# Kernel optimization log

Hardware: AMD Instinct MI355X
Metric: run time of the kernel (lower is better)

Reference implementation:

```python
import jax, jax.numpy as jnp
import numpy as np

SHIFTS = [1, 2, 4]  # matches init_kwargs 'shifts' (all in range 0 < s < channels)


def setup_inputs() -> dict:
    key = jax.random.key(0)
    k1, k2, k3 = jax.random.split(key, 3)
    B, H, L, D = 4, 1, 2048, 512
    factor = 4
    proj_in = 2 * len(SHIFTS) * D  # cli_mode='full' -> 2 components per shift
    x = jax.random.normal(k1, (B, H, L, D), dtype=jnp.float32)
    W = jax.random.normal(k2, (factor, D), dtype=jnp.float32) * 0.05
    # glorot-ish scale for the projection kernel
    proj_kernel = jax.random.normal(k3, (proj_in, D), dtype=jnp.float32) * (1.0 / np.sqrt(proj_in))
    proj_bias = jnp.zeros((D,), dtype=jnp.float32)
    return {"x": x, "W": W, "proj_kernel": proj_kernel, "proj_bias": proj_bias}


def reference(x, W, proj_kernel, proj_bias):
    # x: (B, H, L, D); W: (k, D) slot multivectors
    k, D = W.shape
    B, H, L, _ = x.shape
    # coarse[-1] treated as zeros; non-anchor slots source previous coarse vector
    coarse_prev = jnp.pad(x, ((0, 0), (0, 0), (1, 0), (0, 0)))[:, :, :-1, :]
    # src: (B, H, L, k, D) — slots 0..k-2 from coarse_prev, slot k-1 (anchor) from x
    src = jnp.concatenate(
        [jnp.repeat(coarse_prev[:, :, :, None, :], k - 1, axis=3),
         x[:, :, :, None, :]],
        axis=3,
    )
    W_b = W[None, None, None, :, :]  # (1,1,1,k,D)
    components = []
    for s in SHIFTS:
        src_s = jnp.roll(src, s, axis=-1)
        W_s_b = jnp.roll(W, s, axis=-1)[None, None, None, :, :]
        sw = src * W_s_b
        components.append(sw - W_b * src_s)        # wedge part
        components.append(jax.nn.silu(sw))          # inner part (full mode)
    g = jnp.concatenate(components, axis=-1)  # (B,H,L,k, 2*len(shifts)*D)
    fine = jnp.einsum('bhlkc,cd->bhlkd', g, proj_kernel) + proj_bias
    return fine.reshape(B, H, L * k, D)
```

## Files before the change

### kernel.cpp

```cpp
#include <hip/hip_runtime.h>
#include <cstdint>
#include <cstddef>

#define D_DIM 512
#define L_DIM 2048
#define KB_DIM 2048
#define KS_DIM 1536
#define NROWS_X 2049
#define M_TOT 32768

typedef __bf16 bf16x8 __attribute__((ext_vector_type(8)));
typedef float  f32x4  __attribute__((ext_vector_type(4)));

__device__ __forceinline__ unsigned f2bf(float f) {
  unsigned u = __float_as_uint(f);
  u += 0x7FFF + ((u >> 16) & 1);
  return u >> 16;
}
__device__ __forceinline__ float bf2f(unsigned short u) {
  return __uint_as_float(((unsigned)u) << 16);
}
__device__ __forceinline__ void gld_lds16(const void* g, void* l) {
  __builtin_amdgcn_global_load_lds((const __attribute__((address_space(1))) void*)g,
                                   (__attribute__((address_space(3))) void*)l,
                                   16, 0, 0);
}

__global__ void convert_x(const float* __restrict__ x, unsigned short* __restrict__ XbfZ) {
  const int b = blockIdx.y;
  const int idx = blockIdx.x * 256 + threadIdx.x;
  if (idx >= NROWS_X * 128) return;
  const int rr = idx >> 7;
  const int c4 = idx & 127;
  uint2 p = {0u, 0u};
  if (rr > 0) {
    float4 v = reinterpret_cast<const float4*>(x)[((size_t)b * L_DIM + rr - 1) * 128 + c4];
    p.x = f2bf(v.x) | (f2bf(v.y) << 16);
    p.y = f2bf(v.z) | (f2bf(v.w) << 16);
  }
  reinterpret_cast<uint2*>(XbfZ)[((size_t)b * NROWS_X + rr) * 128 + c4] = p;
}

__global__ void build_B(const float* __restrict__ P, const float* __restrict__ W,
                        unsigned short* __restrict__ Ball,
                        unsigned short* __restrict__ Wtab, int buildWtab) {
  if (buildWtab && blockIdx.x == 0) {
    for (int i = threadIdx.x; i < 6144; i += 256) {
      const int c = i & 511; const int rest = i >> 9;
      const int si = rest % 3; const int jj = rest / 3;
      Wtab[(jj * 3 + si) * 512 + c] =
          (unsigned short)f2bf(W[jj * 512 + ((c - (1 << si)) & 511)]);
    }
  }
  const int bx = blockIdx.x;
  const int j = bx >> 6, dt = (bx >> 3) & 7, ct = bx & 7;
  const int t = threadIdx.x;
  const int d = dt * 64 + (t & 63);
  const int cbase = ct * 64 + (t >> 6) * 16;
  unsigned short bufd[16];
  unsigned short bufs[3][16];
  #pragma unroll
  for (int cc = 0; cc < 16; ++cc) {
    const int c = cbase + cc;
    float qd = 0.f;
    #pragma unroll
    for (int si = 0; si < 3; ++si) {
      const int s = 1 << si;
      const int cm = (c - s) & 511, cp = (c + s) & 511;
      qd += W[j * 512 + cm] * P[((size_t)(2 * si) * 512 + c) * 512 + d]
          - W[j * 512 + cp] * P[((size_t)(2 * si) * 512 + cp) * 512 + d];
      bufs[si][cc] = (unsigned short)f2bf(P[((size_t)(2 * si + 1) * 512 + c) * 512 + d]);
    }
    bufd[cc] = (unsigned short)f2bf(qd);
  }
  unsigned short* row = Ball + (size_t)(j * 512 + d) * KB_DIM;
  *reinterpret_cast<uint4*>(&row[cbase])     = *reinterpret_cast<uint4*>(&bufd[0]);
  *reinterpret_cast<uint4*>(&row[cbase + 8]) = *reinterpret_cast<uint4*>(&bufd[8]);
  #pragma unroll
  for (int si = 0; si < 3; ++si) {
    *reinterpret_cast<uint4*>(&row[512 + si * 512 + cbase])     = *reinterpret_cast<uint4*>(&bufs[si][0]);
    *reinterpret_cast<uint4*>(&row[512 + si * 512 + cbase + 8]) = *reinterpret_cast<uint4*>(&bufs[si][8]);
  }
}

__global__ void gs_gen(const unsigned short* __restrict__ XbfZ,
                       const unsigned short* __restrict__ Wtab,
                       unsigned short* __restrict__ GS) {
  const int m0 = blockIdx.x * 4;
  const int j = m0 >> 13, b = (m0 >> 11) & 3, lbase = m0 & 2047;
  const int r = threadIdx.x >> 6, lane = threadIdx.x & 63;
  const int l = lbase + r;
  const size_t vrow = (size_t)b * NROWS_X + l + (j == 3);
  union U { uint4 q; unsigned short s[8]; };
  U va;
  va.q = *reinterpret_cast<const uint4*>(XbfZ + vrow * 512 + lane * 8);
  unsigned short* o = GS + (size_t)(m0 + r) * KS_DIM + lane * 8;
  #pragma unroll
  for (int si = 0; si < 3; ++si) {
    U wa;
    wa.q = *reinterpret_cast<const uint4*>(Wtab + (j * 3 + si) * 512 + lane * 8);
    unsigned res[4];
    #pragma unroll
    for (int e = 0; e < 4; ++e) {
      float s0 = bf2f(va.s[2 * e])     * bf2f(wa.s[2 * e]);
      float s1 = bf2f(va.s[2 * e + 1]) * bf2f(wa.s[2 * e + 1]);
      float g0 = s0 * __builtin_amdgcn_rcpf(1.f + __expf(-s0));
      float g1 = s1 * __builtin_amdgcn_rcpf(1.f + __expf(-s1));
      res[e] = f2bf(g0) | (f2bf(g1) << 16);
    }
    uint4 ov = {res[0], res[1], res[2], res[3]};
    *reinterpret_cast<uint4*>(o + si * 512) = ov;
  }
}

__global__ __launch_bounds__(256) void gemm_main(
    const unsigned short* __restrict__ XbfZ, const unsigned short* __restrict__ GS,
    const unsigned short* __restrict__ Ball, const float* __restrict__ bias,
    float* __restrict__ out) {
  __shared__ alignas(16) unsigned short At[2][4096];
  __shared__ alignas(16) unsigned short Bt[2][4096];

  const int tid = threadIdx.x;
  const int bx = blockIdx.x;
  const int nt = bx >> 8;
  const int mt = bx & 255;
  const int j  = mt >> 6;
  const int b  = (mt >> 4) & 3;
  const int l0 = (mt & 15) * 128;
  const int n0 = nt * 128;

  const int rA = tid >> 2;
  const int qA = (tid & 3) ^ ((rA >> 2) & 3);
  const unsigned short* srcAd0 = XbfZ + (size_t)(b * NROWS_X + l0 + (j == 3) + rA) * 512 + qA * 8;
  const unsigned short* srcAd1 = srcAd0 + (size_t)64 * 512;
  const size_t mbase = (size_t)((j * 4 + b) * L_DIM + l0);
  const unsigned short* srcAs0 = GS + (mbase + rA) * KS_DIM + qA * 8;
  const unsigned short* srcAs1 = srcAs0 + (size_t)64 * KS_DIM;
  const unsigned short* srcB0 = Ball + (size_t)(j * 512 + n0 + rA) * KB_DIM + qA * 8;
  const unsigned short* srcB1 = srcB0 + (size_t)64 * KB_DIM;

  const int lane = tid & 63, wv = tid >> 6;
  const int wm = wv >> 1, wn = wv & 1;
  const int l16 = lane & 15, quad = lane >> 4;
  const int qf = quad ^ ((l16 >> 2) & 3);
  const int aBase = (wm * 64 + l16) * 32 + qf * 8;
  const int bBase = (wn * 64 + l16) * 32 + qf * 8;

  f32x4 acc[4][4];
  #pragma unroll
  for (int i = 0; i < 4; ++i)
    #pragma unroll
    for (int n = 0; n < 4; ++n)
      acc[i][n] = f32x4{0.f, 0.f, 0.f, 0.f};

  gld_lds16(srcAd0, &At[0][tid * 8]);
  gld_lds16(srcAd1, &At[0][(tid + 256) * 8]);
  gld_lds16(srcB0,  &Bt[0][tid * 8]);
  gld_lds16(srcB1,  &Bt[0][(tid + 256) * 8]);

  for (int it = 0; it < 64; ++it) {
    const int buf = it & 1;
    __syncthreads();
    if (it + 1 < 64) {
      const int nx = it + 1, nb = buf ^ 1;
      const unsigned short *a0, *a1;
      if (nx < 16) { a0 = srcAd0 + nx * 32; a1 = srcAd1 + nx * 32; }
      else { const int o = (nx - 16) * 32; a0 = srcAs0 + o; a1 = srcAs1 + o; }
      gld_lds16(a0, &At[nb][tid * 8]);
      gld_lds16(a1, &At[nb][(tid + 256) * 8]);
      gld_lds16(srcB0 + nx * 32, &Bt[nb][tid * 8]);
      gld_lds16(srcB1 + nx * 32, &Bt[nb][(tid + 256) * 8]);
    }
    bf16x8 af[4], bfr[4];
    #pragma unroll
    for (int mi = 0; mi < 4; ++mi) {
      uint4 rr = *reinterpret_cast<const uint4*>(&At[buf][aBase + mi * 512]);
      af[mi] = __builtin_bit_cast(bf16x8, rr);
    }
    #pragma unroll
    for (int ni = 0; ni < 4; ++ni) {
      uint4 rr = *reinterpret_cast<const uint4*>(&Bt[buf][bBase + ni * 512]);
      bfr[ni] = __builtin_bit_cast(bf16x8, rr);
    }
    #pragma unroll
    for (int mi = 0; mi < 4; ++mi)
      #pragma unroll
      for (int ni = 0; ni < 4; ++ni)
        acc[mi][ni] = __builtin_amdgcn_mfma_f32_16x16x32_bf16(af[mi], bfr[ni], acc[mi][ni], 0, 0, 0);
  }

  #pragma unroll
  for (int ni = 0; ni < 4; ++ni) {
    const int d = n0 + wn * 64 + ni * 16 + l16;
    const float bv = bias[d];
    #pragma unroll
    for (int mi = 0; mi < 4; ++mi) {
      const int lrow = l0 + wm * 64 + mi * 16 + quad * 4;
      #pragma unroll
      for (int rg = 0; rg < 4; ++rg) {
        out[((size_t)(b * L_DIM + lrow + rg) * 4 + j) * D_DIM + d] = acc[mi][ni][rg] + bv;
      }
    }
  }
}

__global__ __launch_bounds__(256, 2) void fused_gemm(
    const unsigned short* __restrict__ XbfZ, const unsigned short* __restrict__ Ball,
    const float* __restrict__ W, const float* __restrict__ bias,
    float* __restrict__ out) {
  __shared__ alignas(16) unsigned short Vt[2][4096];
  __shared__ alignas(16) unsigned short Bt[2][8192];
  __shared__ alignas(16) unsigned short At[128 * 40];
  __shared__ alignas(16) unsigned short Wr[3 * 512];

  const int tid = threadIdx.x;
  const int nt = blockIdx.x & 1;
  const int mt = blockIdx.x >> 1;
  const int j  = mt >> 6;
  const int b  = (mt >> 4) & 3;
  const int lt = mt & 15;
  const int l0 = lt * 128;
  const int n0 = nt * 256;
  const int base_l = l0 - ((j == 3) ? 0 : 1);

  #pragma unroll
  for (int i = 0; i < 6; ++i) {
    const int idx = tid + i * 256;
    const int si = idx >> 9, c = idx & 511, s = 1 << si;
    Wr[idx] = (unsigned short)f2bf(W[j * 512 + ((c - s) & 511)]);
  }

  const int lane = tid & 63, wv = tid >> 6;
  const int qv = (lane & 3) ^ ((lane >> 4) & 3);
  const int rsub = lane >> 2;
  const unsigned short* gA0 = XbfZ + ((size_t)(b * NROWS_X + 1 + base_l + (wv * 2) * 16 + rsub)) * 512 + qv * 8;
  const unsigned short* gA1 = gA0 + (size_t)16 * 512;
  const unsigned short* gB[4];
  #pragma unroll
  for (int pi = 0; pi < 4; ++pi)
    gB[pi] = Ball + (size_t)(j * 512 + n0 + (wv * 4 + pi) * 16 + rsub) * KB_DIM + qv * 8;
  const int vOff0 = wv * 1024 + lane * 8;
  const int bOff0 = wv * 2048 + lane * 8;

  const int am = tid >> 1;
  const int akh = (tid & 1) * 16;
  const int ch0 = (tid & 1) * 2;
  const int sswz = (am >> 2) & 3;
  unsigned short* aDst = &At[am * 40 + akh];

  const int l16 = lane & 15, quad = lane >> 4;
  const int wm = wv >> 1, wn = wv & 1;
  const int fsw = (l16 >> 2) & 3;
  const int aVoff = (wm * 64 + l16) * 32 + ((quad ^ fsw)) * 8;
  const int aSoff = (wm * 64 + l16) * 40 + quad * 8;
  const int bOffF = (wn * 128 + l16) * 32 + ((quad ^ fsw)) * 8;

  f32x4 acc[4][8];
  #pragma unroll
  for (int i = 0; i < 4; ++i)
    #pragma unroll
    for (int n = 0; n < 8; ++n)
      acc[i][n] = f32x4{0.f, 0.f, 0.f, 0.f};

  {
    gld_lds16(gA0, &Vt[0][vOff0]);
    gld_lds16(gA1, &Vt[0][vOff0 + 512]);
    #pragma unroll
    for (int pi = 0; pi < 4; ++pi)
      gld_lds16(gB[pi], &Bt[0][bOff0 + pi * 512]);
  }

  for (int it = 0; it < 64; ++it) {
    const int buf = it & 1;
    const int kk0 = it * 32;
    const int gi = kk0 >> 9;

    __syncthreads();

    if (it + 1 < 64) {
      const int nk = kk0 + 32;
      const int nv = nk & 511;
      gld_lds16(gA0 + nv, &Vt[buf ^ 1][vOff0]);
      gld_lds16(gA1 + nv, &Vt[buf ^ 1][vOff0 + 512]);
      #pragma unroll
      for (int pi = 0; pi < 4; ++pi)
        gld_lds16(gB[pi] + nk, &Bt[buf ^ 1][bOff0 + pi * 512]);
    }

    bf16x8 af[4], bfr[8];
    if (gi == 0) {
      #pragma unroll
      for (int mi = 0; mi < 4; ++mi) {
        uint4 r = *reinterpret_cast<const uint4*>(&Vt[buf][aVoff + mi * 512]);
        af[mi] = __builtin_bit_cast(bf16x8, r);
      }
    } else {
      const int si = gi - 1;
      const int ccbase = (kk0 & 511) + akh;
      uint4 v0 = *reinterpret_cast<const uint4*>(&Vt[buf][(am * 4 + ((ch0)     ^ sswz)) * 8]);
      uint4 v1 = *reinterpret_cast<const uint4*>(&Vt[buf][(am * 4 + ((ch0 + 1) ^ sswz)) * 8]);
      uint4 w0 = *reinterpret_cast<const uint4*>(&Wr[si * 512 + ccbase]);
      uint4 w1 = *reinterpret_cast<const uint4*>(&Wr[si * 512 + ccbase + 8]);
      union U { uint4 q[2]; unsigned short s[16]; };
      U va, wa; va.q[0] = v0; va.q[1] = v1; wa.q[0] = w0; wa.q[1] = w1;
      unsigned res[8];
      #pragma unroll
      for (int e = 0; e < 8; ++e) {
        float s0 = bf2f(va.s[2 * e])     * bf2f(wa.s[2 * e]);
        float s1 = bf2f(va.s[2 * e + 1]) * bf2f(wa.s[2 * e + 1]);
        float g0 = s0 * __builtin_amdgcn_rcpf(1.f + __expf(-s0));
        float g1 = s1 * __builtin_amdgcn_rcpf(1.f + __expf(-s1));
        res[e] = f2bf(g0) | (f2bf(g1) << 16);
      }
      uint4 o0 = {res[0], res[1], res[2], res[3]};
      uint4 o1 = {res[4], res[5], res[6], res[7]};
      *reinterpret_cast<uint4*>(aDst) = o0;
      *reinterpret_cast<uint4*>(aDst + 8) = o1;
      __syncthreads();
      #pragma unroll
      for (int mi = 0; mi < 4; ++mi) {
        uint4 r = *reinterpret_cast<const uint4*>(&At[aSoff + mi * 640]);
        af[mi] = __builtin_bit_cast(bf16x8, r);
      }
    }
    #pragma unroll
    for (int ni = 0; ni < 8; ++ni) {
      uint4 r = *reinterpret_cast<const uint4*>(&Bt[buf][bOffF + ni * 512]);
      bfr[ni] = __builtin_bit_cast(bf16x8, r);
    }
    #pragma unroll
    for (int mi = 0; mi < 4; ++mi)
      #pragma unroll
      for (int ni = 0; ni < 8; ++ni)
        acc[mi][ni] = __builtin_amdgcn_mfma_f32_16x16x32_bf16(af[mi], bfr[ni], acc[mi][ni], 0, 0, 0);
  }

  #pragma unroll
  for (int ni = 0; ni < 8; ++ni) {
    const int d = n0 + wn * 128 + ni * 16 + l16;
    const float bv = bias[d];
    #pragma unroll
    for (int mi = 0; mi < 4; ++mi) {
      const int lrow = l0 + wm * 64 + mi * 16 + quad * 4;
      #pragma unroll
      for (int rg = 0; rg < 4; ++rg) {
        out[((size_t)(b * L_DIM + lrow + rg) * 4 + j) * D_DIM + d] = acc[mi][ni][rg] + bv;
      }
    }
  }
}

extern "C" void kernel_launch(void* const* d_in, const int* in_sizes, int n_in,
                              void* d_out, int out_size, void* d_ws, size_t ws_size,
                              hipStream_t stream) {
  const float* x    = (const float*)d_in[0];
  const float* W    = (const float*)d_in[1];
  const float* P    = (const float*)d_in[2];
  const float* bias = (const float*)d_in[3];
  float* out = (float*)d_out;

  unsigned short* XbfZ = (unsigned short*)d_ws;
  unsigned short* Ball = XbfZ + (size_t)4 * NROWS_X * 512;
  unsigned short* Wtab = Ball + (size_t)4 * 512 * KB_DIM;
  unsigned short* GS   = Wtab + 6144;
  const size_t need_bytes =
      ((size_t)4 * NROWS_X * 512 + (size_t)4 * 512 * KB_DIM + 6144 +
       (size_t)M_TOT * KS_DIM) * 2;
  const bool primary = ws_size >= need_bytes;

  convert_x<<<dim3(1025, 4), 256, 0, stream>>>(x, XbfZ);
  build_B<<<256, 256, 0, stream>>>(P, W, Ball, Wtab, primary ? 1 : 0);
  if (primary) {
    gs_gen<<<8192, 256, 0, stream>>>(XbfZ, Wtab, GS);
    gemm_main<<<1024, 256, 0, stream>>>(XbfZ, GS, Ball, bias, out);
  } else {
    fused_gemm<<<512, 256, 0, stream>>>(XbfZ, Ball, W, bias, out);
  }
}
```

Measured before the change: 195.9 us.

## Replace main GEMM with 256x256-tile 8-wave kernel using ping-pong staged loads

Replaces the 128x128-tile, 4-wave GEMM with a 256x256-tile, 512-thread kernel. Each K step is 64 wide and split into four quarter-phases that interleave LDS reads, async global-to-LDS staging and MFMA bursts under explicit barriers, s_waitcnt and setprio. The grid is also remapped across XCDs. The aim is to raise arithmetic intensity per byte loaded and to overlap memory with MFMA, at the cost of larger LDS use (128KB per block), more accumulator registers and only 256 blocks.

```diff
diff --git a/kernel.cpp b/kernel.cpp
--- a/kernel.cpp
+++ b/kernel.cpp
@@ -113,92 +113,150 @@
   }
 }
 
-__global__ __launch_bounds__(256) void gemm_main(
+#define BARR asm volatile("s_barrier" ::: "memory")
+#define VMW(N) asm volatile("s_waitcnt vmcnt(" #N ")" ::: "memory")
+
+#define READ_A(MH, BUF) do { \
+  _Pragma("unroll") \
+  for (int mf = 0; mf < 4; ++mf) { \
+    a[mf][0] = __builtin_bit_cast(bf16x8, *reinterpret_cast<const uint4*>(&A_lds[BUF][aRow[mf] + (MH)*4096 + p0])); \
+    a[mf][1] = __builtin_bit_cast(bf16x8, *reinterpret_cast<const uint4*>(&A_lds[BUF][aRow[mf] + (MH)*4096 + p1])); \
+  } } while (0)
+
+#define READ_B(NH, BUF, BB) do { \
+  _Pragma("unroll") \
+  for (int nf = 0; nf < 2; ++nf) { \
+    BB[nf][0] = __builtin_bit_cast(bf16x8, *reinterpret_cast<const uint4*>(&B_lds[BUF][bRow[nf] + (NH)*2048 + p0])); \
+    BB[nf][1] = __builtin_bit_cast(bf16x8, *reinterpret_cast<const uint4*>(&B_lds[BUF][bRow[nf] + (NH)*2048 + p1])); \
+  } } while (0)
+
+#define MFMA_Q(MH, NH, BB) do { \
+  _Pragma("unroll") \
+  for (int mf = 0; mf < 4; ++mf) { \
+    _Pragma("unroll") \
+    for (int nf = 0; nf < 2; ++nf) { \
+      acc[(MH)*4+mf][(NH)*2+nf] = __builtin_amdgcn_mfma_f32_16x16x32_bf16(a[mf][0], BB[nf][0], acc[(MH)*4+mf][(NH)*2+nf], 0, 0, 0); \
+      acc[(MH)*4+mf][(NH)*2+nf] = __builtin_amdgcn_mfma_f32_16x16x32_bf16(a[mf][1], BB[nf][1], acc[(MH)*4+mf][(NH)*2+nf], 0, 0, 0); \
+    } } } while (0)
+
+__global__ __launch_bounds__(512, 2) void gemm8(
     const unsigned short* __restrict__ XbfZ, const unsigned short* __restrict__ GS,
     const unsigned short* __restrict__ Ball, const float* __restrict__ bias,
     float* __restrict__ out) {
-  __shared__ alignas(16) unsigned short At[2][4096];
-  __shared__ alignas(16) unsigned short Bt[2][4096];
+  __shared__ alignas(16) unsigned short A_lds[2][16384];
+  __shared__ alignas(16) unsigned short B_lds[2][16384];
 
   const int tid = threadIdx.x;
-  const int bx = blockIdx.x;
-  const int nt = bx >> 8;
-  const int mt = bx & 255;
-  const int j  = mt >> 6;
-  const int b  = (mt >> 4) & 3;
-  const int l0 = (mt & 15) * 128;
-  const int n0 = nt * 128;
-
-  const int rA = tid >> 2;
-  const int qA = (tid & 3) ^ ((rA >> 2) & 3);
-  const unsigned short* srcAd0 = XbfZ + (size_t)(b * NROWS_X + l0 + (j == 3) + rA) * 512 + qA * 8;
-  const unsigned short* srcAd1 = srcAd0 + (size_t)64 * 512;
+  const int bid = blockIdx.x;
+  const int wid = (bid & 7) * 32 + (bid >> 3);
+  const int mtile = wid >> 1;
+  const int ntile = wid & 1;
+  const int j  = mtile >> 5;
+  const int b  = (mtile >> 3) & 3;
+  const int l0 = (mtile & 7) * 256;
+  const int n0 = ntile * 256;
   const size_t mbase = (size_t)((j * 4 + b) * L_DIM + l0);
-  const unsigned short* srcAs0 = GS + (mbase + rA) * KS_DIM + qA * 8;
-  const unsigned short* srcAs1 = srcAs0 + (size_t)64 * KS_DIM;
-  const unsigned short* srcB0 = Ball + (size_t)(j * 512 + n0 + rA) * KB_DIM + qA * 8;
-  const unsigned short* srcB1 = srcB0 + (size_t)64 * KB_DIM;
+
+  const int srow = tid >> 3;
+  const int c8   = (tid & 7) ^ (srow & 7);
+  const unsigned short* pXd = XbfZ + ((size_t)(b * NROWS_X + (j == 3) + l0 + srow)) * 512 + c8 * 8;
+  const unsigned short* pGS = GS + (mbase + srow) * (size_t)KS_DIM + c8 * 8;
+  const unsigned short* pB  = Ball + ((size_t)(j * 512 + n0 + srow)) * KB_DIM + c8 * 8;
+  const int ldsSlot = tid * 8;
+
+  auto stageA = [&](int TT, int h, int bufi) {
+    unsigned short* dst = &A_lds[bufi][h * 8192 + ldsSlot];
+    if (TT < 8) {
+      const unsigned short* s = pXd + (size_t)h * 128 * 512 + TT * 64;
+      gld_lds16(s, dst);
+      gld_lds16(s + 64 * 512, dst + 4096);
+    } else {
+      const unsigned short* s = pGS + (size_t)h * 128 * KS_DIM + (TT - 8) * 64;
+      gld_lds16(s, dst);
+      gld_lds16(s + 64 * KS_DIM, dst + 4096);
+    }
+  };
+  auto stageB = [&](int TT, int h, int bufi) {
+    const unsigned short* s = pB + (size_t)h * 128 * KB_DIM + TT * 64;
+    unsigned short* dst = &B_lds[bufi][h * 8192 + ldsSlot];
+    gld_lds16(s, dst);
+    gld_lds16(s + 64 * KB_DIM, dst + 4096);
+  };
 
   const int lane = tid & 63, wv = tid >> 6;
-  const int wm = wv >> 1, wn = wv & 1;
+  const int wm = wv >> 2, wn = wv & 3;
   const int l16 = lane & 15, quad = lane >> 4;
-  const int qf = quad ^ ((l16 >> 2) & 3);
-  const int aBase = (wm * 64 + l16) * 32 + qf * 8;
-  const int bBase = (wn * 64 + l16) * 32 + qf * 8;
-
-  f32x4 acc[4][4];
-  #pragma unroll
-  for (int i = 0; i < 4; ++i)
+  const int p0 = ((quad)     ^ (l16 & 7)) * 8;
+  const int p1 = ((quad + 4) ^ (l16 & 7)) * 8;
+  int aRow[4], bRow[2];
+  #pragma unroll
+  for (int mf = 0; mf < 4; ++mf) aRow[mf] = (wm * 128 + mf * 16 + l16) * 64;
+  #pragma unroll
+  for (int nf = 0; nf < 2; ++nf) bRow[nf] = (wn * 64 + nf * 16 + l16) * 64;
+
+  f32x4 acc[8][4];
+  #pragma unroll
+  for (int i = 0; i < 8; ++i)
     #pragma unroll
     for (int n = 0; n < 4; ++n)
       acc[i][n] = f32x4{0.f, 0.f, 0.f, 0.f};
 
-  gld_lds16(srcAd0, &At[0][tid * 8]);
-  gld_lds16(srcAd1, &At[0][(tid + 256) * 8]);
-  gld_lds16(srcB0,  &Bt[0][tid * 8]);
-  gld_lds16(srcB1,  &Bt[0][(tid + 256) * 8]);
-
-  for (int it = 0; it < 64; ++it) {
-    const int buf = it & 1;
-    __syncthreads();
-    if (it + 1 < 64) {
-      const int nx = it + 1, nb = buf ^ 1;
-      const unsigned short *a0, *a1;
-      if (nx < 16) { a0 = srcAd0 + nx * 32; a1 = srcAd1 + nx * 32; }
-      else { const int o = (nx - 16) * 32; a0 = srcAs0 + o; a1 = srcAs1 + o; }
-      gld_lds16(a0, &At[nb][tid * 8]);
-      gld_lds16(a1, &At[nb][(tid + 256) * 8]);
-      gld_lds16(srcB0 + nx * 32, &Bt[nb][tid * 8]);
-      gld_lds16(srcB1 + nx * 32, &Bt[nb][(tid + 256) * 8]);
-    }
-    bf16x8 af[4], bfr[4];
-    #pragma unroll
-    for (int mi = 0; mi < 4; ++mi) {
-      uint4 rr = *reinterpret_cast<const uint4*>(&At[buf][aBase + mi * 512]);
-      af[mi] = __builtin_bit_cast(bf16x8, rr);
-    }
-    #pragma unroll
-    for (int ni = 0; ni < 4; ++ni) {
-      uint4 rr = *reinterpret_cast<const uint4*>(&Bt[buf][bBase + ni * 512]);
-      bfr[ni] = __builtin_bit_cast(bf16x8, rr);
-    }
-    #pragma unroll
-    for (int mi = 0; mi < 4; ++mi)
-      #pragma unroll
-      for (int ni = 0; ni < 4; ++ni)
-        acc[mi][ni] = __builtin_amdgcn_mfma_f32_16x16x32_bf16(af[mi], bfr[ni], acc[mi][ni], 0, 0, 0);
-  }
-
-  #pragma unroll
-  for (int ni = 0; ni < 4; ++ni) {
-    const int d = n0 + wn * 64 + ni * 16 + l16;
+  bf16x8 a[4][2], b0[2][2], b1[2][2];
+
+  stageB(0, 0, 0); stageB(0, 1, 0);
+  stageA(0, 0, 0); stageA(0, 1, 0);
+  stageB(1, 0, 1); stageB(1, 1, 1);
+  VMW(4);
+  BARR;
+
+  for (int T = 0; T < 32; ++T) {
+    const int cur = T & 1, nxt = cur ^ 1;
+    READ_A(0, cur);
+    READ_B(0, cur, b0);
+    if (T + 1 < 32) stageA(T + 1, 0, nxt);
+    BARR;
+    __builtin_amdgcn_s_setprio(1);
+    MFMA_Q(0, 0, b0);
+    __builtin_amdgcn_s_setprio(0);
+    BARR;
+    READ_B(1, cur, b1);
+    if (T + 1 < 32) stageA(T + 1, 1, nxt);
+    BARR;
+    __builtin_amdgcn_s_setprio(1);
+    MFMA_Q(0, 1, b1);
+    __builtin_amdgcn_s_setprio(0);
+    BARR;
+    READ_A(1, cur);
+    if (T + 2 < 32) stageB(T + 2, 0, cur);
+    BARR;
+    __builtin_amdgcn_s_setprio(1);
+    MFMA_Q(1, 1, b1);
+    __builtin_amdgcn_s_setprio(0);
+    BARR;
+    if (T + 2 < 32) stageB(T + 2, 1, cur);
+    BARR;
+    __builtin_amdgcn_s_setprio(1);
+    MFMA_Q(1, 0, b0);
+    __builtin_amdgcn_s_setprio(0);
+    if (T < 30) {
+      VMW(4);
+      BARR;
+    } else if (T == 30) {
+      VMW(0);
+      BARR;
+    }
+  }
+
+  #pragma unroll
+  for (int nfg = 0; nfg < 4; ++nfg) {
+    const int d = n0 + wn * 64 + nfg * 16 + l16;
     const float bv = bias[d];
     #pragma unroll
-    for (int mi = 0; mi < 4; ++mi) {
-      const int lrow = l0 + wm * 64 + mi * 16 + quad * 4;
+    for (int mfg = 0; mfg < 8; ++mfg) {
+      const int lrow = l0 + wm * 128 + mfg * 16 + quad * 4;
       #pragma unroll
       for (int rg = 0; rg < 4; ++rg) {
-        out[((size_t)(b * L_DIM + lrow + rg) * 4 + j) * D_DIM + d] = acc[mi][ni][rg] + bv;
+        out[((size_t)(b * L_DIM + lrow + rg) * 4 + j) * D_DIM + d] = acc[mfg][nfg][rg] + bv;
       }
     }
   }
@@ -372,7 +430,7 @@
   build_B<<<256, 256, 0, stream>>>(P, W, Ball, Wtab, primary ? 1 : 0);
   if (primary) {
     gs_gen<<<8192, 256, 0, stream>>>(XbfZ, Wtab, GS);
-    gemm_main<<<1024, 256, 0, stream>>>(XbfZ, GS, Ball, bias, out);
+    gemm8<<<dim3(256), dim3(512), 0, stream>>>(XbfZ, GS, Ball, bias, out);
   } else {
     fused_gemm<<<512, 256, 0, stream>>>(XbfZ, Ball, W, bias, out);
   }
```

Result: faster. 184.1 us (-6.0%).
